# Kernel optimization log

Measured on AMD Instinct MI355X. Metric: run time of the kernel, lower is better.

The kernel has to match this reference:

```python
import jax, jax.numpy as jnp
import numpy as np

NUM_NODES = 50000
INPUT_SIZE = 128
NUM_RELATIONS = 16
NUM_EDGES = 1600000
CLAMP_MIN = 1e-05
CLAMP_MAX = 0.99999


def setup_inputs() -> dict:
    key = jax.random.key(0)
    k1, k2, k3, k4 = jax.random.split(key, 4)
    x = jax.random.normal(k1, (NUM_NODES, INPUT_SIZE), dtype=jnp.float32)
    att_weight = jax.random.normal(k2, (2 * INPUT_SIZE, NUM_RELATIONS), dtype=jnp.float32)
    edge_index = jax.random.randint(k3, (2, NUM_EDGES), 0, NUM_NODES, dtype=jnp.int64)
    edge_type = jax.random.randint(k4, (NUM_EDGES,), 0, NUM_RELATIONS, dtype=jnp.int64)
    return {"x": x, "att_weight": att_weight, "edge_index": edge_index, "edge_type": edge_type}


def reference(x, att_weight, edge_index, edge_type):
    # concat(x[src], x[dst]) @ W  ==  x[src] @ W[:d] + x[dst] @ W[d:]
    d = x.shape[1]
    w_src, w_dst = att_weight[:d], att_weight[d:]
    # logits: [num_edges, num_relations]
    logits = x[edge_index[0]] @ w_src + x[edge_index[1]] @ w_dst
    # select the score for each edge's relation type
    score = jnp.take_along_axis(logits, edge_type[:, None], axis=1)[:, 0]
    att = jax.nn.sigmoid(score)
    return jnp.clip(att, CLAMP_MIN, CLAMP_MAX)
```

## Files before the change

### kernel.cpp

```cpp
#include <hip/hip_runtime.h>
#include <hip/hip_fp16.h>

#define INPUT_SIZE 128
#define NUM_REL 16

typedef int   i32x4 __attribute__((ext_vector_type(4)));
typedef float f32x4 __attribute__((ext_vector_type(4)));

__global__ __launch_bounds__(256) void node_logits_kernel(
    const float* __restrict__ x,
    const float* __restrict__ w,
    __half* __restrict__ Ls,
    __half* __restrict__ Ld,
    int num_nodes)
{
    __shared__ float swc[128 * 32];

    const int tid = threadIdx.x;

    #pragma unroll
    for (int i = 0; i < 16; ++i) {
        const int idx = i * 256 + tid;
        const int k = idx >> 5, r = idx & 31;
        swc[idx] = (r < 16) ? w[k * NUM_REL + r]
                            : w[(INPUT_SIZE + k) * NUM_REL + (r - 16)];
    }
    __syncthreads();

    const int ng = tid >> 3;
    const int rg = tid & 7;
    const int node0 = blockIdx.x * 128 + ng * 4;
    const int r0 = rg * 4;

    const f32x4* xr[4];
    bool valid[4];
    #pragma unroll
    for (int n = 0; n < 4; ++n) {
        const int nn = node0 + n;
        valid[n] = (nn < num_nodes);
        xr[n] = (const f32x4*)(x + (size_t)(valid[n] ? nn : 0) * INPUT_SIZE);
    }

    float acc[4][4] = {};

    #pragma unroll 4
    for (int ks = 0; ks < 32; ++ks) {
        f32x4 xv[4], wv[4];
        #pragma unroll
        for (int n = 0; n < 4; ++n) xv[n] = xr[n][ks];
        #pragma unroll
        for (int kk = 0; kk < 4; ++kk)
            wv[kk] = *(const f32x4*)&swc[(ks * 4 + kk) * 32 + r0];

        #pragma unroll
        for (int n = 0; n < 4; ++n) {
            #pragma unroll
            for (int c = 0; c < 4; ++c) {
                acc[n][0] += xv[n][c] * wv[c][0];
                acc[n][1] += xv[n][c] * wv[c][1];
                acc[n][2] += xv[n][c] * wv[c][2];
                acc[n][3] += xv[n][c] * wv[c][3];
            }
        }
    }

    __half* base = (rg < 4) ? Ls : Ld;
    const int rr = (rg & 3) * 4;
    #pragma unroll
    for (int n = 0; n < 4; ++n) {
        if (!valid[n]) continue;
        union { __half2 h2[2]; uint2 u; } pk;
        pk.h2[0] = __floats2half2_rn(acc[n][0], acc[n][1]);
        pk.h2[1] = __floats2half2_rn(acc[n][2], acc[n][3]);
        *(uint2*)(base + (size_t)(node0 + n) * NUM_REL + rr) = pk.u;
    }
}

__global__ __launch_bounds__(256) void edge_score_kernel(
    const int* __restrict__ ei,
    const int* __restrict__ et,
    const __half* __restrict__ Ls,
    const __half* __restrict__ Ld,
    float* __restrict__ out,
    int num_edges)
{
    const int i = blockIdx.x * blockDim.x + threadIdx.x;
    if (i * 2 >= num_edges) return;

    const int2 s2 = ((const int2*)ei)[i];
    const int2 d2 = ((const int2*)(ei + num_edges))[i];
    const int2 t2 = ((const int2*)et)[i];

    const __half a0 = Ls[(size_t)s2.x * NUM_REL + t2.x];
    const __half a1 = Ls[(size_t)s2.y * NUM_REL + t2.y];
    const __half b0 = Ld[(size_t)d2.x * NUM_REL + t2.x];
    const __half b1 = Ld[(size_t)d2.y * NUM_REL + t2.y];

    const float sc0 = __half2float(a0) + __half2float(b0);
    const float sc1 = __half2float(a1) + __half2float(b1);
    const float r0 = fminf(fmaxf(1.f / (1.f + __expf(-sc0)), 1e-5f), 0.99999f);
    const float r1 = fminf(fmaxf(1.f / (1.f + __expf(-sc1)), 1e-5f), 0.99999f);

    ((float2*)out)[i] = make_float2(r0, r1);
}

__global__ void edge_direct_kernel(const float* __restrict__ x,
                                   const float* __restrict__ w,
                                   const int* __restrict__ ei,
                                   const int* __restrict__ et,
                                   float* __restrict__ out,
                                   int num_edges) {
    const int e = blockIdx.x * blockDim.x + threadIdx.x;
    if (e >= num_edges) return;
    const int s = ei[e];
    const int d = ei[num_edges + e];
    const int t = et[e];
    const float* xs = x + (size_t)s * INPUT_SIZE;
    const float* xd = x + (size_t)d * INPUT_SIZE;
    float acc = 0.f;
    #pragma unroll 4
    for (int k = 0; k < INPUT_SIZE; ++k)
        acc += xs[k] * w[k * NUM_REL + t] + xd[k] * w[(INPUT_SIZE + k) * NUM_REL + t];
    const float att = 1.f / (1.f + __expf(-acc));
    out[e] = fminf(fmaxf(att, 1e-5f), 0.99999f);
}

extern "C" void kernel_launch(void* const* d_in, const int* in_sizes, int n_in,
                              void* d_out, int out_size, void* d_ws, size_t ws_size,
                              hipStream_t stream) {
    const float* x  = (const float*)d_in[0];
    const float* w  = (const float*)d_in[1];
    const int*   ei = (const int*)d_in[2];
    const int*   et = (const int*)d_in[3];
    float* out = (float*)d_out;

    const int num_nodes = in_sizes[0] / INPUT_SIZE;
    const int num_edges = in_sizes[3];

    const size_t tbl_bytes = (size_t)num_nodes * NUM_REL * sizeof(__half);
    const size_t ws_needed = 2 * tbl_bytes;

    if (ws_size >= ws_needed && (num_edges & 1) == 0) {
        __half* Ls = (__half*)d_ws;
        __half* Ld = (__half*)((char*)d_ws + tbl_bytes);

        const int blocks1 = (num_nodes + 127) / 128;
        node_logits_kernel<<<blocks1, 256, 0, stream>>>(x, w, Ls, Ld, num_nodes);

        const int pairs   = num_edges / 2;
        const int blocks2 = (pairs + 255) / 256;
        edge_score_kernel<<<blocks2, 256, 0, stream>>>(ei, et, Ls, Ld, out, num_edges);
    } else {
        const int blocks = (num_edges + 255) / 256;
        edge_direct_kernel<<<blocks, 256, 0, stream>>>(x, w, ei, et, out, num_edges);
    }
}
```

Before: 43.84 us.

## Split edge scoring into node-range partitioned source and destination passes

Replaces the single edge scoring kernel with four passes. Two source passes each gather Ls entries for edges whose source node lies in one half of the node range and write fp16 partial sums to a workspace buffer. Two destination passes then add the Ld entries over the same halves and apply sigmoid and clamp. The aim is to shrink the working set of each gather so the table stays cache-resident. The cost is reading the index arrays four times, an extra partial-sum buffer round trip, more kernel launches, and divergent half-empty threads.

```diff
diff --git a/kernel.cpp b/kernel.cpp
--- a/kernel.cpp
+++ b/kernel.cpp
@@ -76,32 +76,53 @@
     }
 }
 
-__global__ __launch_bounds__(256) void edge_score_kernel(
+__global__ __launch_bounds__(256) void edge_src_pass(
     const int* __restrict__ ei,
     const int* __restrict__ et,
     const __half* __restrict__ Ls,
-    const __half* __restrict__ Ld,
-    float* __restrict__ out,
-    int num_edges)
+    __half* __restrict__ partial,
+    int num_edges, int lo, int hi)
 {
     const int i = blockIdx.x * blockDim.x + threadIdx.x;
-    if (i * 2 >= num_edges) return;
+    const int e0 = i * 4;
+    if (e0 >= num_edges) return;
 
-    const int2 s2 = ((const int2*)ei)[i];
-    const int2 d2 = ((const int2*)(ei + num_edges))[i];
-    const int2 t2 = ((const int2*)et)[i];
+    const i32x4 s4 = ((const i32x4*)ei)[i];
+    const i32x4 t4 = ((const i32x4*)et)[i];
 
-    const __half a0 = Ls[(size_t)s2.x * NUM_REL + t2.x];
-    const __half a1 = Ls[(size_t)s2.y * NUM_REL + t2.y];
-    const __half b0 = Ld[(size_t)d2.x * NUM_REL + t2.x];
-    const __half b1 = Ld[(size_t)d2.y * NUM_REL + t2.y];
+    #pragma unroll
+    for (int j = 0; j < 4; ++j) {
+        const int s = s4[j];
+        if (s >= lo && s < hi)
+            partial[e0 + j] = Ls[(size_t)s * NUM_REL + t4[j]];
+    }
+}
 
-    const float sc0 = __half2float(a0) + __half2float(b0);
-    const float sc1 = __half2float(a1) + __half2float(b1);
-    const float r0 = fminf(fmaxf(1.f / (1.f + __expf(-sc0)), 1e-5f), 0.99999f);
-    const float r1 = fminf(fmaxf(1.f / (1.f + __expf(-sc1)), 1e-5f), 0.99999f);
+__global__ __launch_bounds__(256) void edge_dst_pass(
+    const int* __restrict__ ei,
+    const int* __restrict__ et,
+    const __half* __restrict__ Ld,
+    const __half* __restrict__ partial,
+    float* __restrict__ out,
+    int num_edges, int lo, int hi)
+{
+    const int i = blockIdx.x * blockDim.x + threadIdx.x;
+    const int e0 = i * 4;
+    if (e0 >= num_edges) return;
 
-    ((float2*)out)[i] = make_float2(r0, r1);
+    const i32x4 d4 = ((const i32x4*)(ei + num_edges))[i];
+    const i32x4 t4 = ((const i32x4*)et)[i];
+
+    #pragma unroll
+    for (int j = 0; j < 4; ++j) {
+        const int d = d4[j];
+        if (d >= lo && d < hi) {
+            const float sc = __half2float(partial[e0 + j])
+                           + __half2float(Ld[(size_t)d * NUM_REL + t4[j]]);
+            const float att = 1.f / (1.f + __expf(-sc));
+            out[e0 + j] = fminf(fmaxf(att, 1e-5f), 0.99999f);
+        }
+    }
 }
 
 __global__ void edge_direct_kernel(const float* __restrict__ x,
@@ -138,18 +159,29 @@
     const int num_edges = in_sizes[3];
 
     const size_t tbl_bytes = (size_t)num_nodes * NUM_REL * sizeof(__half);
-    const size_t ws_needed = 2 * tbl_bytes;
+    const size_t par_bytes = (size_t)num_edges * sizeof(__half);
+    const size_t ws_needed = 2 * tbl_bytes + par_bytes;
 
-    if (ws_size >= ws_needed && (num_edges & 1) == 0) {
-        __half* Ls = (__half*)d_ws;
-        __half* Ld = (__half*)((char*)d_ws + tbl_bytes);
+    if (ws_size >= ws_needed && (num_edges & 3) == 0) {
+        __half* Ls      = (__half*)d_ws;
+        __half* Ld      = (__half*)((char*)d_ws + tbl_bytes);
+        __half* partial = (__half*)((char*)d_ws + 2 * tbl_bytes);
 
         const int blocks1 = (num_nodes + 127) / 128;
         node_logits_kernel<<<blocks1, 256, 0, stream>>>(x, w, Ls, Ld, num_nodes);
 
-        const int pairs   = num_edges / 2;
-        const int blocks2 = (pairs + 255) / 256;
-        edge_score_kernel<<<blocks2, 256, 0, stream>>>(ei, et, Ls, Ld, out, num_edges);
+        const int quads   = num_edges / 4;
+        const int blocks2 = (quads + 255) / 256;
+        const int mid     = num_nodes / 2;
+
+        edge_src_pass<<<blocks2, 256, 0, stream>>>(ei, et, Ls, partial,
+                                                   num_edges, 0, mid);
+        edge_src_pass<<<blocks2, 256, 0, stream>>>(ei, et, Ls, partial,
+                                                   num_edges, mid, num_nodes);
+        edge_dst_pass<<<blocks2, 256, 0, stream>>>(ei, et, Ld, partial, out,
+                                                   num_edges, 0, mid);
+        edge_dst_pass<<<blocks2, 256, 0, stream>>>(ei, et, Ld, partial, out,
+                                                   num_edges, mid, num_nodes);
     } else {
         const int blocks = (num_edges + 255) / 256;
         edge_direct_kernel<<<blocks, 256, 0, stream>>>(x, w, ei, et, out, num_edges);
```

Measured after the change: 55.60 us. 1.27x slower.
